# Kernel tuning notes

Measured on AMD Instinct MI355X. Metric: run time of the kernel, lower is better.

Reference implementation:

```python
import jax, jax.numpy as jnp
import numpy as np

B, S, D, H, NH = 128, 512, 64, 256, 8
HD = H // NH
NEG = -10000000000.0


def _ln(x, g, b, eps=1e-5):
    m = x.mean(-1, keepdims=True)
    v = ((x - m) ** 2).mean(-1, keepdims=True)
    return (x - m) * jax.lax.rsqrt(v + eps) * g + b


def _mha(xq, xkv, mask, qW, qb, kW, kb, vW, vb, oW, ob):
    # mask: [B,1,1,S_kv] bool, True = masked out
    b, sq, _ = xq.shape
    sk = xkv.shape[1]
    Q = (xq @ qW + qb).reshape(b, sq, NH, HD).transpose(0, 2, 1, 3)
    K = (xkv @ kW + kb).reshape(b, sk, NH, HD).transpose(0, 2, 1, 3)
    V = (xkv @ vW + vb).reshape(b, sk, NH, HD).transpose(0, 2, 1, 3)
    energy = jnp.einsum('bhqd,bhkd->bhqk', Q, K) / jnp.sqrt(jnp.float32(HD))
    energy = jnp.where(mask, NEG, energy)
    attn = jax.nn.softmax(energy, axis=-1)  # dropout is identity in eval
    x = jnp.einsum('bhqk,bhkd->bhqd', attn, V)
    x = x.transpose(0, 2, 1, 3).reshape(b, sq, H)
    return x @ oW + ob


def _ffn(x, f1W, f1b, f2W, f2b):
    # NewGELU == tanh-approximate GELU (GPT-2)
    return jax.nn.gelu(x @ f1W + f1b, approximate=True) @ f2W + f2b


def _fwd(src, ln0sg, ln0sb, ln0tg, ln0tb, semW, semb, temW, temb,
         e_qW, e_qb, e_kW, e_kb, e_vW, e_vb, e_oW, e_ob, e_ln1g, e_ln1b,
         e_f1W, e_f1b, e_f2W, e_f2b, e_ln2g, e_ln2b,
         d_sqW, d_sqb, d_skW, d_skb, d_svW, d_svb, d_soW, d_sob, d_ln1g, d_ln1b,
         d_eqW, d_eqb, d_ekW, d_ekb, d_evW, d_evb, d_eoW, d_eob, d_ln2g, d_ln2b,
         d_f1W, d_f1b, d_f2W, d_f2b, d_ln3g, d_ln3b, outW, outb):
    valid = src.sum(-1) != 0                      # [B,S] (prod_fea == 0)
    amask = (~valid)[:, None, None, :]            # [B,1,1,S]; trg==src so trg_mask==src_mask
    embs_src = _ln(src, ln0sg, ln0sb) @ semW + semb   # emb_need
    embs_trg = _ln(src, ln0tg, ln0tb) @ temW + temb
    # encoder layer
    a = _mha(embs_src, embs_src, amask, e_qW, e_qb, e_kW, e_kb, e_vW, e_vb, e_oW, e_ob)
    x = _ln(embs_src + a, e_ln1g, e_ln1b)
    enc_src = _ln(x + _ffn(x, e_f1W, e_f1b, e_f2W, e_f2b), e_ln2g, e_ln2b)
    # decoder layer
    a = _mha(embs_trg, embs_trg, amask, d_sqW, d_sqb, d_skW, d_skb, d_svW, d_svb, d_soW, d_sob)
    t = _ln(embs_trg + a, d_ln1g, d_ln1b)
    a = _mha(t, enc_src, amask, d_eqW, d_eqb, d_ekW, d_ekb, d_evW, d_evb, d_eoW, d_eob)
    t = _ln(t + a, d_ln2g, d_ln2b)
    t = _ln(t + _ffn(t, d_f1W, d_f1b, d_f2W, d_f2b), d_ln3g, d_ln3b)
    logits = (t @ outW + outb)[..., 0]            # [B,S]
    p = jnp.exp(logits) * valid.astype(logits.dtype)
    return p / p.sum(-1, keepdims=True)           # multi_purchase=False branch


def setup_inputs() -> dict:
    key = jax.random.key(0)
    keys = iter(jax.random.split(key, 64))
    inp = {"src": jax.random.normal(next(keys), (B, S, D), dtype=jnp.float32)}

    def lin(name, i, o):
        inp[name + "W"] = jax.random.normal(next(keys), (i, o), dtype=jnp.float32) * 0.02
        inp[name + "b"] = jnp.zeros((o,), dtype=jnp.float32)

    def ln(name, d):
        inp[name + "g"] = jnp.ones((d,), dtype=jnp.float32)
        inp[name + "b"] = jnp.zeros((d,), dtype=jnp.float32)

    ln("ln0s", D); ln("ln0t", D)
    lin("sem", D, H); lin("tem", D, H)
    for n in ["e_q", "e_k", "e_v", "e_o"]:
        lin(n, H, H)
    ln("e_ln1", H); lin("e_f1", H, H); lin("e_f2", H, H); ln("e_ln2", H)
    for n in ["d_sq", "d_sk", "d_sv", "d_so", "d_eq", "d_ek", "d_ev", "d_eo"]:
        lin(n, H, H)
    ln("d_ln1", H); ln("d_ln2", H)
    lin("d_f1", H, H); lin("d_f2", H, H); ln("d_ln3", H)
    lin("out", H, 1)
    return inp


def reference(src, ln0sg, ln0sb, ln0tg, ln0tb, semW, semb, temW, temb,
              e_qW, e_qb, e_kW, e_kb, e_vW, e_vb, e_oW, e_ob, e_ln1g, e_ln1b,
              e_f1W, e_f1b, e_f2W, e_f2b, e_ln2g, e_ln2b,
              d_sqW, d_sqb, d_skW, d_skb, d_svW, d_svb, d_soW, d_sob, d_ln1g, d_ln1b,
              d_eqW, d_eqb, d_ekW, d_ekb, d_evW, d_evb, d_eoW, d_eob, d_ln2g, d_ln2b,
              d_f1W, d_f1b, d_f2W, d_f2b, d_ln3g, d_ln3b, outW, outb):
    return _fwd(src, ln0sg, ln0sb, ln0tg, ln0tb, semW, semb, temW, temb,
                e_qW, e_qb, e_kW, e_kb, e_vW, e_vb, e_oW, e_ob, e_ln1g, e_ln1b,
                e_f1W, e_f1b, e_f2W, e_f2b, e_ln2g, e_ln2b,
                d_sqW, d_sqb, d_skW, d_skb, d_svW, d_svb, d_soW, d_sob, d_ln1g, d_ln1b,
                d_eqW, d_eqb, d_ekW, d_ekb, d_evW, d_evb, d_eoW, d_eob, d_ln2g, d_ln2b,
                d_f1W, d_f1b, d_f2W, d_f2b, d_ln3g, d_ln3b, outW, outb)
```

## Files before the change

### kernel.cpp

```cpp
#include <hip/hip_runtime.h>
#include <hip/hip_bf16.h>


#define Bb  128
#define Ss  512
#define Hh  256
#define NHh 8
#define Mm  (Bb*Ss)

typedef unsigned short bf16_t;
typedef __attribute__((ext_vector_type(8))) short short8;
typedef __attribute__((ext_vector_type(4))) float f32x4;

__device__ __forceinline__ float bf2f(bf16_t h){
  union { unsigned int u; float f; } v; v.u = ((unsigned int)h)<<16; return v.f;
}
__device__ __forceinline__ bf16_t f2bf(float f){
  union { float f; unsigned int u; } v; v.f = f;
  unsigned int r = (v.u + 0x7fffu + ((v.u>>16)&1u)) >> 16;
  return (bf16_t)r;
}
__device__ __forceinline__ unsigned pk_bf16(float a, float b){
  union { __hip_bfloat162 h; unsigned u; } v;
  v.h = __float22bfloat162_rn(float2{a,b});
  return v.u;
}
__device__ __forceinline__ short8 ld_bf8(const bf16_t* p){
  union { uint4 u; short8 s; } v; v.u = *(const uint4*)p; return v.s;
}
__device__ __forceinline__ void gload16(const bf16_t* g, bf16_t* l){
  __builtin_amdgcn_global_load_lds(
      (const __attribute__((address_space(1))) void*)g,
      (__attribute__((address_space(3))) void*)l, 16, 0, 0);
}
__device__ __forceinline__ float exp2_hw(float x){
  float r; asm("v_exp_f32 %0, %1" : "=v"(r) : "v"(x)); return r;
}
__device__ __forceinline__ float gelu_f(float x){
  float u = 0.7978845608028654f*(x + 0.044715f*x*x*x);
  float e = __expf(2.0f*u);
  float th = 1.0f - 2.0f*__builtin_amdgcn_rcpf(e + 1.0f);
  return 0.5f*x*(1.0f + th);
}

struct PrepDesc { const float* s; unsigned off; int K; };
struct Prep18  { PrepDesc d[18]; };

__global__ __launch_bounds__(256) void k_prep(Prep18 p, bf16_t* __restrict__ arena)
{
  PrepDesc dd = p.d[blockIdx.y];
  int i = blockIdx.x*256 + threadIdx.x;
  if (i < dd.K*256){
    int k = i>>8, n = i&255;
    arena[dd.off + n*dd.K + k] = f2bf(dd.s[i]);
  }
}

__global__ __launch_bounds__(256) void k_ln0(const float* __restrict__ src,
    const float* __restrict__ gs, const float* __restrict__ bs,
    const float* __restrict__ gt, const float* __restrict__ bt,
    bf16_t* __restrict__ xs, bf16_t* __restrict__ xt, float* __restrict__ valid)
{
  int row  = blockIdx.x*4 + (threadIdx.x>>6);
  int lane = threadIdx.x & 63;
  float x = src[(size_t)row*64 + lane];
  float s = x;
  #pragma unroll
  for (int o=32;o>0;o>>=1) s += __shfl_xor(s,o);
  float mean = s*(1.0f/64.0f);
  float d = x - mean;
  float ss = d*d;
  #pragma unroll
  for (int o=32;o>0;o>>=1) ss += __shfl_xor(ss,o);
  float r = rsqrtf(ss*(1.0f/64.0f) + 1e-5f);
  float xn = d*r;
  xs[(size_t)row*64+lane] = f2bf(xn*gs[lane] + bs[lane]);
  xt[(size_t)row*64+lane] = f2bf(xn*gt[lane] + bt[lane]);
  if (lane==0) valid[row] = (s != 0.0f) ? 1.0f : 0.0f;
}

struct GemmJob  { const bf16_t* A; const bf16_t* Wt; const float* bias; bf16_t* C;
                  int outm; float cs; };
struct GemmJobs { GemmJob j[3]; };

template<int KK>
__global__ __launch_bounds__(256,4) void k_gemm3(GemmJobs jobs)
{
  __shared__ bf16_t As[8*512];
  __shared__ bf16_t Bs[32*512];
  GemmJob jb = jobs.j[blockIdx.y];
  int t = threadIdx.x, w = t>>6, lane = t&63, l15 = lane&15, quad = lane>>4;
  int m0 = blockIdx.x*64;
  f32x4 z = {0.f,0.f,0.f,0.f};
  f32x4 acc[4][4] = {{z,z,z,z},{z,z,z,z},{z,z,z,z},{z,z,z,z}};

  #pragma unroll
  for (int k0=0; k0<KK; k0+=64){
    #pragma unroll
    for (int j=0; j<2; j++){
      int id = 2*w + j; int kc32 = id>>2, mt = id&3;
      gload16(jb.A + (size_t)(m0 + mt*16 + l15)*KK + k0 + kc32*32 + quad*8,
              &As[id*512]);
    }
    #pragma unroll
    for (int j=0; j<8; j++){
      int id = 8*w + j; int kc32 = id>>4, gnt = id&15;
      gload16(jb.Wt + (size_t)(gnt*16 + l15)*KK + k0 + kc32*32 + quad*8,
              &Bs[id*512]);
    }
    __syncthreads();
    #pragma unroll
    for (int kc=0; kc<2; kc++){
      short8 a[4], b[4];
      #pragma unroll
      for (int mt=0; mt<4; mt++) a[mt] = ld_bf8(&As[(kc*4+mt)*512 + lane*8]);
      #pragma unroll
      for (int nt=0; nt<4; nt++) b[nt] = ld_bf8(&Bs[(kc*16 + w*4 + nt)*512 + lane*8]);
      #pragma unroll
      for (int mt=0; mt<4; mt++)
        #pragma unroll
        for (int nt=0; nt<4; nt++)
          acc[mt][nt] = __builtin_amdgcn_mfma_f32_16x16x32_bf16(a[mt], b[nt], acc[mt][nt], 0,0,0);
    }
    __syncthreads();
  }

  float bv[4];
  #pragma unroll
  for (int nt=0; nt<4; nt++) bv[nt] = jb.bias[w*64 + nt*16 + l15];
  float cs = jb.cs;

  if (jb.outm == 0){
    #pragma unroll
    for (int mt=0; mt<4; mt++)
      #pragma unroll
      for (int nt=0; nt<4; nt++){
        int m = m0 + mt*16 + quad*4;
        int col = w*64 + nt*16 + l15;
        #pragma unroll
        for (int r=0; r<4; r++)
          jb.C[(size_t)(m+r)*256 + col] = f2bf((acc[mt][nt][r] + bv[nt])*cs);
      }
  } else {
    #pragma unroll
    for (int mt=0; mt<4; mt++)
      #pragma unroll
      for (int nt=0; nt<4; nt++){
        int m = m0 + mt*16 + quad*4;
        int col = w*64 + nt*16 + l15;
        uint2 pk = { pk_bf16(acc[mt][nt][0]+bv[nt], acc[mt][nt][1]+bv[nt]),
                     pk_bf16(acc[mt][nt][2]+bv[nt], acc[mt][nt][3]+bv[nt]) };
        *(uint2*)&jb.C[((size_t)((m>>9)*256 + col))*512 + (m&511)] = pk;
      }
  }
}

struct QkvJob { const bf16_t* A;
                const bf16_t* Wt0; const bf16_t* Wt1; const bf16_t* Wt2;
                const float* b0; const float* b1; const float* b2;
                bf16_t* C0; bf16_t* C1; bf16_t* C2; float qs; };

__global__ __launch_bounds__(256,2) void k_qkv(QkvJob jb)
{
  __shared__ bf16_t As[32*512];
  __shared__ bf16_t Bs[32*512];
  int t = threadIdx.x, w = t>>6, lane = t&63, l15 = lane&15, quad = lane>>4;
  int m0 = blockIdx.x*64;
  f32x4 z = {0.f,0.f,0.f,0.f};

  #pragma unroll
  for (int j=0; j<8; j++){
    int id = 8*w + j; int kc32 = id>>2, mt = id&3;
    gload16(jb.A + (size_t)(m0 + mt*16 + l15)*256 + kc32*32 + quad*8,
            &As[id*512]);
  }

  const bf16_t* Wts[3]  = { jb.Wt0, jb.Wt1, jb.Wt2 };
  const float*  bias[3] = { jb.b0,  jb.b1,  jb.b2  };
  bf16_t*       Cs[3]   = { jb.C0,  jb.C1,  jb.C2  };

  #pragma unroll 1
  for (int o=0; o<3; o++){
    const bf16_t* Wt = Wts[o];
    f32x4 acc[4][4] = {{z,z,z,z},{z,z,z,z},{z,z,z,z},{z,z,z,z}};
    #pragma unroll 1
    for (int ki=0; ki<4; ki++){
      #pragma unroll
      for (int j=0; j<8; j++){
        int id = 8*w + j; int kc32 = id>>4, gnt = id&15;
        gload16(Wt + (size_t)(gnt*16 + l15)*256 + ki*64 + kc32*32 + quad*8,
                &Bs[id*512]);
      }
      __syncthreads();
      #pragma unroll
      for (int kc=0; kc<2; kc++){
        short8 a[4], b[4];
        #pragma unroll
        for (int mt=0; mt<4; mt++)
          a[mt] = ld_bf8(&As[((ki*2+kc)*4 + mt)*512 + lane*8]);
        #pragma unroll
        for (int nt=0; nt<4; nt++)
          b[nt] = ld_bf8(&Bs[(kc*16 + w*4 + nt)*512 + lane*8]);
        #pragma unroll
        for (int mt=0; mt<4; mt++)
          #pragma unroll
          for (int nt=0; nt<4; nt++)
            acc[mt][nt] = __builtin_amdgcn_mfma_f32_16x16x32_bf16(a[mt], b[nt], acc[mt][nt], 0,0,0);
      }
      __syncthreads();
    }
    float bv[4];
    #pragma unroll
    for (int nt=0; nt<4; nt++) bv[nt] = bias[o][w*64 + nt*16 + l15];
    bf16_t* C = Cs[o];
    if (o < 2){
      float cs = (o==0) ? jb.qs : 1.0f;
      #pragma unroll
      for (int mt=0; mt<4; mt++)
        #pragma unroll
        for (int nt=0; nt<4; nt++){
          int m = m0 + mt*16 + quad*4;
          int col = w*64 + nt*16 + l15;
          #pragma unroll
          for (int r=0; r<4; r++)
            C[(size_t)(m+r)*256 + col] = f2bf((acc[mt][nt][r] + bv[nt])*cs);
        }
    } else {
      #pragma unroll
      for (int mt=0; mt<4; mt++)
        #pragma unroll
        for (int nt=0; nt<4; nt++){
          int m = m0 + mt*16 + quad*4;
          int col = w*64 + nt*16 + l15;
          uint2 pk = { pk_bf16(acc[mt][nt][0]+bv[nt], acc[mt][nt][1]+bv[nt]),
                       pk_bf16(acc[mt][nt][2]+bv[nt], acc[mt][nt][3]+bv[nt]) };
          *(uint2*)&C[((size_t)((m>>9)*256 + col))*512 + (m&511)] = pk;
        }
    }
  }
}

template<int EPI, int OUTM, int KK>
__global__ __launch_bounds__(256,4) void k_gemm(const bf16_t* __restrict__ A,
    const bf16_t* __restrict__ Wt, const float* __restrict__ bias,
    void* __restrict__ Cv, const bf16_t* __restrict__ Pres,
    const float* __restrict__ g, const float* __restrict__ bb,
    const float* __restrict__ oW, const float* __restrict__ obp)
{
  __shared__ bf16_t As[8*512];
  __shared__ bf16_t Bs[32*512];
  int t = threadIdx.x, w = t>>6, lane = t&63, l15 = lane&15, quad = lane>>4;
  int m0 = blockIdx.x*64;
  f32x4 z = {0.f,0.f,0.f,0.f};
  f32x4 acc[4][4] = {{z,z,z,z},{z,z,z,z},{z,z,z,z},{z,z,z,z}};

  #pragma unroll
  for (int k0=0; k0<KK; k0+=64){
    #pragma unroll
    for (int j=0; j<2; j++){
      int id = 2*w + j; int kc32 = id>>2, mt = id&3;
      gload16(A + (size_t)(m0 + mt*16 + l15)*KK + k0 + kc32*32 + quad*8,
              &As[id*512]);
    }
    #pragma unroll
    for (int j=0; j<8; j++){
      int id = 8*w + j; int kc32 = id>>4, gnt = id&15;
      gload16(Wt + (size_t)(gnt*16 + l15)*KK + k0 + kc32*32 + quad*8,
              &Bs[id*512]);
    }
    __syncthreads();
    #pragma unroll
    for (int kc=0; kc<2; kc++){
      short8 a[4], b[4];
      #pragma unroll
      for (int mt=0; mt<4; mt++) a[mt] = ld_bf8(&As[(kc*4+mt)*512 + lane*8]);
      #pragma unroll
      for (int nt=0; nt<4; nt++) b[nt] = ld_bf8(&Bs[(kc*16 + w*4 + nt)*512 + lane*8]);
      #pragma unroll
      for (int mt=0; mt<4; mt++)
        #pragma unroll
        for (int nt=0; nt<4; nt++)
          acc[mt][nt] = __builtin_amdgcn_mfma_f32_16x16x32_bf16(a[mt], b[nt], acc[mt][nt], 0,0,0);
    }
    __syncthreads();
  }

  float bv[4];
  #pragma unroll
  for (int nt=0; nt<4; nt++) bv[nt] = bias[w*64 + nt*16 + l15];

  if (OUTM==0){
    #pragma unroll
    for (int mt=0; mt<4; mt++)
      #pragma unroll
      for (int nt=0; nt<4; nt++)
        #pragma unroll
        for (int r=0; r<4; r++){
          int row = m0 + mt*16 + quad*4 + r;
          int col = w*64 + nt*16 + l15;
          float v = acc[mt][nt][r] + bv[nt];
          if (EPI==1) v = gelu_f(v);
          ((bf16_t*)Cv)[(size_t)row*256 + col] = f2bf(v);
        }
  } else {
    float* RedS = (float*)As;
    float* RedQ = RedS + 256;
    #pragma unroll
    for (int mt=0; mt<4; mt++)
      #pragma unroll
      for (int r=0; r<4; r++){
        int row = m0 + mt*16 + quad*4 + r;
        const bf16_t* pr = Pres + (size_t)row*256;
        float s = 0.f, q = 0.f;
        #pragma unroll
        for (int nt=0; nt<4; nt++){
          float v = acc[mt][nt][r] + bv[nt] + bf2f(pr[w*64 + nt*16 + l15]);
          s += v; q += v*v;
        }
        s += __shfl_xor(s,1); s += __shfl_xor(s,2);
        s += __shfl_xor(s,4); s += __shfl_xor(s,8);
        q += __shfl_xor(q,1); q += __shfl_xor(q,2);
        q += __shfl_xor(q,4); q += __shfl_xor(q,8);
        if (l15==0){
          int rr = mt*16 + quad*4 + r;
          RedS[rr*4 + w] = s; RedQ[rr*4 + w] = q;
        }
      }
    __syncthreads();

    float gv[4], bbv[4], wv[4];
    #pragma unroll
    for (int nt=0; nt<4; nt++){ gv[nt] = g[w*64+nt*16+l15]; bbv[nt] = bb[w*64+nt*16+l15]; }
    if (OUTM==5)
      #pragma unroll
      for (int nt=0; nt<4; nt++) wv[nt] = oW[w*64+nt*16+l15];

    float s2p[4][4];
    #pragma unroll
    for (int mt=0; mt<4; mt++)
      #pragma unroll
      for (int r=0; r<4; r++){
        int rr = mt*16 + quad*4 + r;
        int row = m0 + rr;
        float S = RedS[rr*4+0]+RedS[rr*4+1]+RedS[rr*4+2]+RedS[rr*4+3];
        float Q = RedQ[rr*4+0]+RedQ[rr*4+1]+RedQ[rr*4+2]+RedQ[rr*4+3];
        float mean = S*(1.0f/256.0f);
        float var  = Q*(1.0f/256.0f) - mean*mean;
        float rstd = rsqrtf(var + 1e-5f);
        const bf16_t* pr = Pres + (size_t)row*256;
        if (OUTM==3){
          bf16_t* po = (bf16_t*)Cv + (size_t)row*256;
          #pragma unroll
          for (int nt=0; nt<4; nt++){
            float v = acc[mt][nt][r] + bv[nt] + bf2f(pr[w*64 + nt*16 + l15]);
            po[w*64 + nt*16 + l15] = f2bf((v-mean)*rstd*gv[nt] + bbv[nt]);
          }
        } else {
          float s2 = 0.f;
          #pragma unroll
          for (int nt=0; nt<4; nt++){
            float v = acc[mt][nt][r] + bv[nt] + bf2f(pr[w*64 + nt*16 + l15]);
            s2 += ((v-mean)*rstd*gv[nt] + bbv[nt]) * wv[nt];
          }
          s2 += __shfl_xor(s2,1); s2 += __shfl_xor(s2,2);
          s2 += __shfl_xor(s2,4); s2 += __shfl_xor(s2,8);
          s2p[mt][r] = s2;
        }
      }
    if (OUTM==5){
      __syncthreads();
      #pragma unroll
      for (int mt=0; mt<4; mt++)
        #pragma unroll
        for (int r=0; r<4; r++)
          if (l15==0) RedS[(mt*16 + quad*4 + r)*4 + w] = s2p[mt][r];
      __syncthreads();
      if (w==0){
        float S = RedS[lane*4+0]+RedS[lane*4+1]+RedS[lane*4+2]+RedS[lane*4+3];
        ((float*)Cv)[m0 + lane] = S + obp[0];
      }
    }
  }
}

__global__ __launch_bounds__(256) void k_attn(const bf16_t* __restrict__ Qm,
    const bf16_t* __restrict__ Km, const bf16_t* __restrict__ VT,
    const float* __restrict__ valid, bf16_t* __restrict__ AO)
{
  __shared__ bf16_t Pbuf[4][2][2][16][40];
  __shared__ float  Smask[512];
  int t = threadIdx.x, wave = t>>6, lane = t&63, l15 = lane&15, quad = lane>>4;
  int lid = blockIdx.x + 8*blockIdx.y + 1024*blockIdx.z;
  int hp = lid & 3, pb = (lid>>2)&1, g = (lid>>3)&7, bh = lid>>6;
  int h  = hp*2 + (g&1);
  int qc = g>>1;
  int b  = bh*2 + pb;
  int q0 = qc*128;

  Smask[t]     = (valid[b*Ss + t      ] != 0.f) ? 0.f : -1.44269504e10f;
  Smask[t+256] = (valid[b*Ss + t + 256] != 0.f) ? 0.f : -1.44269504e10f;
  __syncthreads();

  short8 aQ0 = ld_bf8(Qm + (size_t)(b*Ss + q0 + (wave*2  )*16 + l15)*256 + h*32 + quad*8);
  short8 aQ1 = ld_bf8(Qm + (size_t)(b*Ss + q0 + (wave*2+1)*16 + l15)*256 + h*32 + quad*8);
  const bf16_t* Kb = Km + (size_t)(b*Ss)*256 + h*32;
  const bf16_t* Vb = VT + ((size_t)b*256 + h*32)*512;

  f32x4 z = {0.f,0.f,0.f,0.f};
  f32x4 O0[2] = {z,z}, O1[2] = {z,z};
  float ls0 = 0.f, ls1 = 0.f;

  auto process = [&](int kt2n, short8 K0, short8 K1){
    int s = kt2n & 1;
    #pragma unroll
    for (int half=0; half<2; half++){
      short8 aK = half ? K1 : K0;
      int ktile = kt2n*2 + half;
      __builtin_amdgcn_s_setprio(1);
      f32x4 s0 = __builtin_amdgcn_mfma_f32_16x16x32_bf16(aK, aQ0, z, 0,0,0);
      f32x4 s1 = __builtin_amdgcn_mfma_f32_16x16x32_bf16(aK, aQ1, z, 0,0,0);
      __builtin_amdgcn_s_setprio(0);
      float4 mb = *(const float4*)&Smask[ktile*16 + quad*4];
      float p00 = exp2_hw(s0[0] + mb.x);
      float p01 = exp2_hw(s0[1] + mb.y);
      float p02 = exp2_hw(s0[2] + mb.z);
      float p03 = exp2_hw(s0[3] + mb.w);
      float p10 = exp2_hw(s1[0] + mb.x);
      float p11 = exp2_hw(s1[1] + mb.y);
      float p12 = exp2_hw(s1[2] + mb.z);
      float p13 = exp2_hw(s1[3] + mb.w);
      ls0 += (p00+p01)+(p02+p03);
      ls1 += (p10+p11)+(p12+p13);
      uint2 w0 = { pk_bf16(p00,p01), pk_bf16(p02,p03) };
      uint2 w1 = { pk_bf16(p10,p11), pk_bf16(p12,p13) };
      *(uint2*)&Pbuf[wave][0][s][l15][half*16 + quad*4] = w0;
      *(uint2*)&Pbuf[wave][1][s][l15][half*16 + quad*4] = w1;
    }
  };
  auto loadK = [&](int n, short8& K0, short8& K1){
    K0 = ld_bf8(Kb + (size_t)((n*2  )*16 + l15)*256 + quad*8);
    K1 = ld_bf8(Kb + (size_t)((n*2+1)*16 + l15)*256 + quad*8);
  };
  auto loadV = [&](int n, short8& V0, short8& V1){
    V0 = ld_bf8(Vb + (size_t)(l15   )*512 + n*32 + quad*8);
    V1 = ld_bf8(Vb + (size_t)(16+l15)*512 + n*32 + quad*8);
  };

  short8 cK0, cK1, pK0, pK1, nK0, nK1;
  short8 cV0, cV1, mV0, mV1, nV0, nV1;
  loadK(0, cK0, cK1);
  process(0, cK0, cK1);
  loadK(1, pK0, pK1);
  loadV(0, cV0, cV1);
  loadV(1, mV0, mV1);

  #pragma unroll 2
  for (int kt2=0; kt2<16; kt2++){
    if (kt2+2 < 16){ loadK(kt2+2, nK0, nK1); loadV(kt2+2, nV0, nV1); }
    int s = kt2 & 1;
    short8 aP0 = ld_bf8(&Pbuf[wave][0][s][l15][quad*8]);
    short8 aP1 = ld_bf8(&Pbuf[wave][1][s][l15][quad*8]);
    __builtin_amdgcn_s_setprio(1);
    O0[0] = __builtin_amdgcn_mfma_f32_16x16x32_bf16(aP0, cV0, O0[0], 0,0,0);
    O0[1] = __builtin_amdgcn_mfma_f32_16x16x32_bf16(aP0, cV1, O0[1], 0,0,0);
    O1[0] = __builtin_amdgcn_mfma_f32_16x16x32_bf16(aP1, cV0, O1[0], 0,0,0);
    O1[1] = __builtin_amdgcn_mfma_f32_16x16x32_bf16(aP1, cV1, O1[1], 0,0,0);
    __builtin_amdgcn_s_setprio(0);
    if (kt2+1 < 16) process(kt2+1, pK0, pK1);
    pK0 = nK0; pK1 = nK1;
    cV0 = mV0; cV1 = mV1; mV0 = nV0; mV1 = nV1;
  }

  ls0 += __shfl_xor(ls0,16); ls0 += __shfl_xor(ls0,32);
  ls1 += __shfl_xor(ls1,16); ls1 += __shfl_xor(ls1,32);
  float linv0 = (ls0 > 0.f) ? 1.0f/ls0 : 0.f;
  float linv1 = (ls1 > 0.f) ? 1.0f/ls1 : 0.f;
  float i0[4], i1[4];
  #pragma unroll
  for (int r=0; r<4; r++){
    i0[r] = __shfl(linv0, quad*4 + r);
    i1[r] = __shfl(linv1, quad*4 + r);
  }
  size_t r0 = (size_t)(b*Ss + q0 + (wave*2  )*16);
  size_t r1 = (size_t)(b*Ss + q0 + (wave*2+1)*16);
  #pragma unroll
  for (int nt=0; nt<2; nt++)
    #pragma unroll
    for (int r=0; r<4; r++){
      AO[(r0 + quad*4 + r)*256 + h*32 + nt*16 + l15] = f2bf(O0[nt][r]*i0[r]);
      AO[(r1 + quad*4 + r)*256 + h*32 + nt*16 + l15] = f2bf(O1[nt][r]*i1[r]);
    }
}

__global__ __launch_bounds__(256) void k_final(const float* __restrict__ L,
    const float* __restrict__ valid, float* __restrict__ out)
{
  __shared__ float wsum[4];
  int b = blockIdx.x, t = threadIdx.x;
  float e0 = __expf(L[b*Ss + t      ]) * valid[b*Ss + t      ];
  float e1 = __expf(L[b*Ss + 256 + t]) * valid[b*Ss + 256 + t];
  float s = e0 + e1;
  #pragma unroll
  for (int o=32;o>0;o>>=1) s += __shfl_xor(s,o);
  if ((t&63)==0) wsum[t>>6] = s;
  __syncthreads();
  float tot = wsum[0]+wsum[1]+wsum[2]+wsum[3];
  out[b*Ss + t      ] = e0/tot;
  out[b*Ss + 256 + t] = e1/tot;
}

extern "C" void kernel_launch(void* const* d_in, const int* in_sizes, int n_in,
                              void* d_out, int out_size, void* d_ws, size_t ws_size,
                              hipStream_t stream)
{
  #define F(i) ((const float*)d_in[(i)])
  bool sig = (in_sizes[33] == 256);
  const float* d_eqW  = F(sig?35:33); const float* d_eqb  = F(sig?36:34);
  const float* d_ekW  = F(sig?37:35); const float* d_ekb  = F(sig?38:36);
  const float* d_evW  = F(sig?39:37); const float* d_evb  = F(sig?40:38);
  const float* d_eoW  = F(sig?41:39); const float* d_eob  = F(sig?42:40);
  const float* d_ln1g = F(sig?33:41); const float* d_ln1b = F(sig?34:42);

  char* w = (char*)d_ws;
  bf16_t* P0 = (bf16_t*)w; w += (size_t)Mm*Hh*2;
  bf16_t* P1 = (bf16_t*)w; w += (size_t)Mm*Hh*2;
  bf16_t* H0 = (bf16_t*)w; w += (size_t)Mm*Hh*2;
  bf16_t* H1 = (bf16_t*)w;
  bf16_t* xs = (bf16_t*)w; w += (size_t)Mm*Hh*2;
  bf16_t* H2 = (bf16_t*)w;
  bf16_t* xt = (bf16_t*)w; w += (size_t)Mm*Hh*2;
  bf16_t* Wa = (bf16_t*)w; w += (size_t)(2*16384 + 16*65536)*2;
  float*  valid  = (float*)w; w += (size_t)Mm*4;
  float*  logits = (float*)w; w += (size_t)Mm*4;
  float* out = (float*)d_out;

  unsigned o_sem = 0, o_tem = 16384;
  unsigned o_w[16]; for (int i=0;i<16;i++) o_w[i] = 32768 + i*65536u;
  Prep18 pp;
  const float* srcs[18] = { F(5), F(7), F(9), F(11), F(13), F(15), F(19), F(21),
                            F(25), F(27), F(29), F(31), d_eqW, d_ekW, d_evW, d_eoW,
                            F(45), F(47) };
  unsigned offs[18] = { o_sem, o_tem, o_w[0],o_w[1],o_w[2],o_w[3],o_w[4],o_w[5],
                        o_w[6],o_w[7],o_w[8],o_w[9],o_w[10],o_w[11],o_w[12],o_w[13],
                        o_w[14],o_w[15] };
  for (int i=0;i<18;i++){ pp.d[i].s = srcs[i]; pp.d[i].off = offs[i]; pp.d[i].K = (i<2)?64:256; }

  dim3 blk(256);
  dim3 gLN(Mm/4);
  dim3 gG(Mm/64);
  dim3 gA(NHh, Bb, 4);
  dim3 gP(256, 18);
  const float* NF = nullptr; const bf16_t* NB = nullptr;
  const float QS = 0.17677669529663687f * 1.4426950408889634f;

  k_prep<<<gP, blk, 0, stream>>>(pp, Wa);
  k_ln0<<<gLN, blk, 0, stream>>>(F(0), F(1),F(2), F(3),F(4), xs, xt, valid);

  {
    GemmJobs js;
    js.j[0] = { xs, Wa+o_sem, F(6), P0, 0, 1.0f };
    js.j[1] = { xt, Wa+o_tem, F(8), P1, 0, 1.0f };
    js.j[2] = js.j[0];
    k_gemm3<64><<<dim3(Mm/64,2), blk, 0, stream>>>(js);
  }

  auto QJ = [&](const bf16_t* A, int wq, int wk, int wv,
                const float* bq, const float* bk, const float* bv2,
                const bf16_t* Ak){
    QkvJob j; j.A = A;
    j.Wt0 = Wa+o_w[wq]; j.Wt1 = Wa+o_w[wk]; j.Wt2 = Wa+o_w[wv];
    j.b0 = bq; j.b1 = bk; j.b2 = bv2;
    j.C0 = H0; j.C1 = H1; j.C2 = H2; j.qs = QS;
    (void)Ak; return j;
  };

  {
    QkvJob j = QJ(P0, 0,1,2, F(10),F(12),F(14), P0);
    k_qkv<<<gG, blk, 0, stream>>>(j);
  }
  k_attn<<<gA, blk, 0, stream>>>(H0, H1, H2, valid, H0);
  k_gemm<0,3,256><<<gG, blk, 0, stream>>>(H0, Wa+o_w[3], F(16), P0, P0, F(17),F(18), NF,NF);
  k_gemm<1,0,256><<<gG, blk, 0, stream>>>(P0, Wa+o_w[4], F(20), H0, NB,NF,NF,NF,NF);
  k_gemm<0,3,256><<<gG, blk, 0, stream>>>(H0, Wa+o_w[5], F(22), P0, P0, F(23),F(24), NF,NF);

  {
    QkvJob j = QJ(P1, 6,7,8, F(26),F(28),F(30), P1);
    k_qkv<<<gG, blk, 0, stream>>>(j);
  }
  k_attn<<<gA, blk, 0, stream>>>(H0, H1, H2, valid, H0);
  k_gemm<0,3,256><<<gG, blk, 0, stream>>>(H0, Wa+o_w[9], F(32), P1, P1, d_ln1g,d_ln1b, NF,NF);

  {
    k_gemm<0,0,256><<<gG, blk, 0, stream>>>(P1, Wa+o_w[10], d_eqb, H0, NB,NF,NF,NF,NF);
    GemmJobs js;
    js.j[0] = { P0, Wa+o_w[11], d_ekb, H1, 0, 1.0f };
    js.j[1] = { P0, Wa+o_w[12], d_evb, H2, 2, 1.0f };
    js.j[2] = js.j[0];
    k_gemm3<256><<<dim3(Mm/64,2), blk, 0, stream>>>(js);
  }
  k_attn<<<gA, blk, 0, stream>>>(H0, H1, H2, valid, H0);
  k_gemm<0,3,256><<<gG, blk, 0, stream>>>(H0, Wa+o_w[13], d_eob, P1, P1, F(43),F(44), NF,NF);

  k_gemm<1,0,256><<<gG, blk, 0, stream>>>(P1, Wa+o_w[14], F(46), H0, NB,NF,NF,NF,NF);
  k_gemm<0,5,256><<<gG, blk, 0, stream>>>(H0, Wa+o_w[15], F(48), logits, P1, F(49),F(50), F(51),F(52));

  k_final<<<dim3(Bb), blk, 0, stream>>>(logits, valid, out);
  #undef F
}
```

Baseline: 1.020 ms.

## Use 128-row GEMM tiles with 512-thread blocks to share weight tiles

Doubles the M tile of the generic and triple-job GEMM kernels from 64 to 128 rows and runs them with 8 waves per block, arranged as 2 row halves by 4 column groups. Each 256-wide weight tile loaded into shared memory is now reused across twice as many rows, which halves weight traffic per output row and halves the grid size. The fused residual+LayerNorm and logit epilogues are reworked to reduce across the new wave layout. Block-level occupancy and register limits change with the 512-thread launch bounds.

```diff
diff --git a/kernel.cpp b/kernel.cpp
--- a/kernel.cpp
+++ b/kernel.cpp
@@ -84,13 +84,14 @@
 struct GemmJobs { GemmJob j[3]; };
 
 template<int KK>
-__global__ __launch_bounds__(256,4) void k_gemm3(GemmJobs jobs)
-{
-  __shared__ bf16_t As[8*512];
+__global__ __launch_bounds__(512,6) void k_gemm3(GemmJobs jobs)
+{
+  __shared__ bf16_t As[16*512];
   __shared__ bf16_t Bs[32*512];
   GemmJob jb = jobs.j[blockIdx.y];
   int t = threadIdx.x, w = t>>6, lane = t&63, l15 = lane&15, quad = lane>>4;
-  int m0 = blockIdx.x*64;
+  int wh = w>>2, wn = w&3;
+  int m0 = blockIdx.x*128;
   f32x4 z = {0.f,0.f,0.f,0.f};
   f32x4 acc[4][4] = {{z,z,z,z},{z,z,z,z},{z,z,z,z},{z,z,z,z}};
 
@@ -98,13 +99,13 @@
   for (int k0=0; k0<KK; k0+=64){
     #pragma unroll
     for (int j=0; j<2; j++){
-      int id = 2*w + j; int kc32 = id>>2, mt = id&3;
-      gload16(jb.A + (size_t)(m0 + mt*16 + l15)*KK + k0 + kc32*32 + quad*8,
+      int id = 2*w + j; int h = id>>3, kc32 = (id>>2)&1, mt = id&3;
+      gload16(jb.A + (size_t)(m0 + h*64 + mt*16 + l15)*KK + k0 + kc32*32 + quad*8,
               &As[id*512]);
     }
     #pragma unroll
-    for (int j=0; j<8; j++){
-      int id = 8*w + j; int kc32 = id>>4, gnt = id&15;
+    for (int j=0; j<4; j++){
+      int id = 4*w + j; int kc32 = id>>4, gnt = id&15;
       gload16(jb.Wt + (size_t)(gnt*16 + l15)*KK + k0 + kc32*32 + quad*8,
               &Bs[id*512]);
     }
@@ -113,9 +114,9 @@
     for (int kc=0; kc<2; kc++){
       short8 a[4], b[4];
       #pragma unroll
-      for (int mt=0; mt<4; mt++) a[mt] = ld_bf8(&As[(kc*4+mt)*512 + lane*8]);
-      #pragma unroll
-      for (int nt=0; nt<4; nt++) b[nt] = ld_bf8(&Bs[(kc*16 + w*4 + nt)*512 + lane*8]);
+      for (int mt=0; mt<4; mt++) a[mt] = ld_bf8(&As[(wh*8 + kc*4 + mt)*512 + lane*8]);
+      #pragma unroll
+      for (int nt=0; nt<4; nt++) b[nt] = ld_bf8(&Bs[(kc*16 + wn*4 + nt)*512 + lane*8]);
       #pragma unroll
       for (int mt=0; mt<4; mt++)
         #pragma unroll
@@ -127,7 +128,7 @@
 
   float bv[4];
   #pragma unroll
-  for (int nt=0; nt<4; nt++) bv[nt] = jb.bias[w*64 + nt*16 + l15];
+  for (int nt=0; nt<4; nt++) bv[nt] = jb.bias[wn*64 + nt*16 + l15];
   float cs = jb.cs;
 
   if (jb.outm == 0){
@@ -135,8 +136,8 @@
     for (int mt=0; mt<4; mt++)
       #pragma unroll
       for (int nt=0; nt<4; nt++){
-        int m = m0 + mt*16 + quad*4;
-        int col = w*64 + nt*16 + l15;
+        int m = m0 + wh*64 + mt*16 + quad*4;
+        int col = wn*64 + nt*16 + l15;
         #pragma unroll
         for (int r=0; r<4; r++)
           jb.C[(size_t)(m+r)*256 + col] = f2bf((acc[mt][nt][r] + bv[nt])*cs);
@@ -146,8 +147,8 @@
     for (int mt=0; mt<4; mt++)
       #pragma unroll
       for (int nt=0; nt<4; nt++){
-        int m = m0 + mt*16 + quad*4;
-        int col = w*64 + nt*16 + l15;
+        int m = m0 + wh*64 + mt*16 + quad*4;
+        int col = wn*64 + nt*16 + l15;
         uint2 pk = { pk_bf16(acc[mt][nt][0]+bv[nt], acc[mt][nt][1]+bv[nt]),
                      pk_bf16(acc[mt][nt][2]+bv[nt], acc[mt][nt][3]+bv[nt]) };
         *(uint2*)&jb.C[((size_t)((m>>9)*256 + col))*512 + (m&511)] = pk;
@@ -241,16 +242,17 @@
 }
 
 template<int EPI, int OUTM, int KK>
-__global__ __launch_bounds__(256,4) void k_gemm(const bf16_t* __restrict__ A,
+__global__ __launch_bounds__(512,6) void k_gemm(const bf16_t* __restrict__ A,
     const bf16_t* __restrict__ Wt, const float* __restrict__ bias,
     void* __restrict__ Cv, const bf16_t* __restrict__ Pres,
     const float* __restrict__ g, const float* __restrict__ bb,
     const float* __restrict__ oW, const float* __restrict__ obp)
 {
-  __shared__ bf16_t As[8*512];
+  __shared__ bf16_t As[16*512];
   __shared__ bf16_t Bs[32*512];
   int t = threadIdx.x, w = t>>6, lane = t&63, l15 = lane&15, quad = lane>>4;
-  int m0 = blockIdx.x*64;
+  int wh = w>>2, wn = w&3;
+  int m0 = blockIdx.x*128;
   f32x4 z = {0.f,0.f,0.f,0.f};
   f32x4 acc[4][4] = {{z,z,z,z},{z,z,z,z},{z,z,z,z},{z,z,z,z}};
 
@@ -258,13 +260,13 @@
   for (int k0=0; k0<KK; k0+=64){
     #pragma unroll
     for (int j=0; j<2; j++){
-      int id = 2*w + j; int kc32 = id>>2, mt = id&3;
-      gload16(A + (size_t)(m0 + mt*16 + l15)*KK + k0 + kc32*32 + quad*8,
+      int id = 2*w + j; int h = id>>3, kc32 = (id>>2)&1, mt = id&3;
+      gload16(A + (size_t)(m0 + h*64 + mt*16 + l15)*KK + k0 + kc32*32 + quad*8,
               &As[id*512]);
     }
     #pragma unroll
-    for (int j=0; j<8; j++){
-      int id = 8*w + j; int kc32 = id>>4, gnt = id&15;
+    for (int j=0; j<4; j++){
+      int id = 4*w + j; int kc32 = id>>4, gnt = id&15;
       gload16(Wt + (size_t)(gnt*16 + l15)*KK + k0 + kc32*32 + quad*8,
               &Bs[id*512]);
     }
@@ -273,9 +275,9 @@
     for (int kc=0; kc<2; kc++){
       short8 a[4], b[4];
       #pragma unroll
-      for (int mt=0; mt<4; mt++) a[mt] = ld_bf8(&As[(kc*4+mt)*512 + lane*8]);
-      #pragma unroll
-      for (int nt=0; nt<4; nt++) b[nt] = ld_bf8(&Bs[(kc*16 + w*4 + nt)*512 + lane*8]);
+      for (int mt=0; mt<4; mt++) a[mt] = ld_bf8(&As[(wh*8 + kc*4 + mt)*512 + lane*8]);
+      #pragma unroll
+      for (int nt=0; nt<4; nt++) b[nt] = ld_bf8(&Bs[(kc*16 + wn*4 + nt)*512 + lane*8]);
       #pragma unroll
       for (int mt=0; mt<4; mt++)
         #pragma unroll
@@ -287,7 +289,7 @@
 
   float bv[4];
   #pragma unroll
-  for (int nt=0; nt<4; nt++) bv[nt] = bias[w*64 + nt*16 + l15];
+  for (int nt=0; nt<4; nt++) bv[nt] = bias[wn*64 + nt*16 + l15];
 
   if (OUTM==0){
     #pragma unroll
@@ -296,51 +298,49 @@
       for (int nt=0; nt<4; nt++)
         #pragma unroll
         for (int r=0; r<4; r++){
-          int row = m0 + mt*16 + quad*4 + r;
-          int col = w*64 + nt*16 + l15;
+          int row = m0 + wh*64 + mt*16 + quad*4 + r;
+          int col = wn*64 + nt*16 + l15;
           float v = acc[mt][nt][r] + bv[nt];
           if (EPI==1) v = gelu_f(v);
           ((bf16_t*)Cv)[(size_t)row*256 + col] = f2bf(v);
         }
   } else {
     float* RedS = (float*)As;
-    float* RedQ = RedS + 256;
+    float* RedQ = RedS + 512;
     #pragma unroll
     for (int mt=0; mt<4; mt++)
       #pragma unroll
       for (int r=0; r<4; r++){
-        int row = m0 + mt*16 + quad*4 + r;
+        int rr = wh*64 + mt*16 + quad*4 + r;
+        int row = m0 + rr;
         const bf16_t* pr = Pres + (size_t)row*256;
         float s = 0.f, q = 0.f;
         #pragma unroll
         for (int nt=0; nt<4; nt++){
-          float v = acc[mt][nt][r] + bv[nt] + bf2f(pr[w*64 + nt*16 + l15]);
+          float v = acc[mt][nt][r] + bv[nt] + bf2f(pr[wn*64 + nt*16 + l15]);
           s += v; q += v*v;
         }
         s += __shfl_xor(s,1); s += __shfl_xor(s,2);
         s += __shfl_xor(s,4); s += __shfl_xor(s,8);
         q += __shfl_xor(q,1); q += __shfl_xor(q,2);
         q += __shfl_xor(q,4); q += __shfl_xor(q,8);
-        if (l15==0){
-          int rr = mt*16 + quad*4 + r;
-          RedS[rr*4 + w] = s; RedQ[rr*4 + w] = q;
-        }
+        if (l15==0){ RedS[rr*4 + wn] = s; RedQ[rr*4 + wn] = q; }
       }
     __syncthreads();
 
     float gv[4], bbv[4], wv[4];
     #pragma unroll
-    for (int nt=0; nt<4; nt++){ gv[nt] = g[w*64+nt*16+l15]; bbv[nt] = bb[w*64+nt*16+l15]; }
+    for (int nt=0; nt<4; nt++){ gv[nt] = g[wn*64+nt*16+l15]; bbv[nt] = bb[wn*64+nt*16+l15]; }
     if (OUTM==5)
       #pragma unroll
-      for (int nt=0; nt<4; nt++) wv[nt] = oW[w*64+nt*16+l15];
+      for (int nt=0; nt<4; nt++) wv[nt] = oW[wn*64+nt*16+l15];
 
     float s2p[4][4];
     #pragma unroll
     for (int mt=0; mt<4; mt++)
       #pragma unroll
       for (int r=0; r<4; r++){
-        int rr = mt*16 + quad*4 + r;
+        int rr = wh*64 + mt*16 + quad*4 + r;
         int row = m0 + rr;
         float S = RedS[rr*4+0]+RedS[rr*4+1]+RedS[rr*4+2]+RedS[rr*4+3];
         float Q = RedQ[rr*4+0]+RedQ[rr*4+1]+RedQ[rr*4+2]+RedQ[rr*4+3];
@@ -352,14 +352,14 @@
           bf16_t* po = (bf16_t*)Cv + (size_t)row*256;
           #pragma unroll
           for (int nt=0; nt<4; nt++){
-            float v = acc[mt][nt][r] + bv[nt] + bf2f(pr[w*64 + nt*16 + l15]);
-            po[w*64 + nt*16 + l15] = f2bf((v-mean)*rstd*gv[nt] + bbv[nt]);
+            float v = acc[mt][nt][r] + bv[nt] + bf2f(pr[wn*64 + nt*16 + l15]);
+            po[wn*64 + nt*16 + l15] = f2bf((v-mean)*rstd*gv[nt] + bbv[nt]);
           }
         } else {
           float s2 = 0.f;
           #pragma unroll
           for (int nt=0; nt<4; nt++){
-            float v = acc[mt][nt][r] + bv[nt] + bf2f(pr[w*64 + nt*16 + l15]);
+            float v = acc[mt][nt][r] + bv[nt] + bf2f(pr[wn*64 + nt*16 + l15]);
             s2 += ((v-mean)*rstd*gv[nt] + bbv[nt]) * wv[nt];
           }
           s2 += __shfl_xor(s2,1); s2 += __shfl_xor(s2,2);
@@ -373,11 +373,12 @@
       for (int mt=0; mt<4; mt++)
         #pragma unroll
         for (int r=0; r<4; r++)
-          if (l15==0) RedS[(mt*16 + quad*4 + r)*4 + w] = s2p[mt][r];
+          if (l15==0) RedS[(wh*64 + mt*16 + quad*4 + r)*4 + wn] = s2p[mt][r];
       __syncthreads();
-      if (w==0){
-        float S = RedS[lane*4+0]+RedS[lane*4+1]+RedS[lane*4+2]+RedS[lane*4+3];
-        ((float*)Cv)[m0 + lane] = S + obp[0];
+      if (w < 2){
+        int rr = w*64 + lane;
+        float S = RedS[rr*4+0]+RedS[rr*4+1]+RedS[rr*4+2]+RedS[rr*4+3];
+        ((float*)Cv)[m0 + rr] = S + obp[0];
       }
     }
   }
@@ -546,8 +547,10 @@
   for (int i=0;i<18;i++){ pp.d[i].s = srcs[i]; pp.d[i].off = offs[i]; pp.d[i].K = (i<2)?64:256; }
 
   dim3 blk(256);
+  dim3 blk512(512);
   dim3 gLN(Mm/4);
   dim3 gG(Mm/64);
+  dim3 gG2(Mm/128);
   dim3 gA(NHh, Bb, 4);
   dim3 gP(256, 18);
   const float* NF = nullptr; const bf16_t* NB = nullptr;
@@ -561,7 +564,7 @@
     js.j[0] = { xs, Wa+o_sem, F(6), P0, 0, 1.0f };
     js.j[1] = { xt, Wa+o_tem, F(8), P1, 0, 1.0f };
     js.j[2] = js.j[0];
-    k_gemm3<64><<<dim3(Mm/64,2), blk, 0, stream>>>(js);
+    k_gemm3<64><<<dim3(Mm/128,2), blk512, 0, stream>>>(js);
   }
 
   auto QJ = [&](const bf16_t* A, int wq, int wk, int wv,
@@ -579,30 +582,30 @@
     k_qkv<<<gG, blk, 0, stream>>>(j);
   }
   k_attn<<<gA, blk, 0, stream>>>(H0, H1, H2, valid, H0);
-  k_gemm<0,3,256><<<gG, blk, 0, stream>>>(H0, Wa+o_w[3], F(16), P0, P0, F(17),F(18), NF,NF);
-  k_gemm<1,0,256><<<gG, blk, 0, stream>>>(P0, Wa+o_w[4], F(20), H0, NB,NF,NF,NF,NF);
-  k_gemm<0,3,256><<<gG, blk, 0, stream>>>(H0, Wa+o_w[5], F(22), P0, P0, F(23),F(24), NF,NF);
+  k_gemm<0,3,256><<<gG2, blk512, 0, stream>>>(H0, Wa+o_w[3], F(16), P0, P0, F(17),F(18), NF,NF);
+  k_gemm<1,0,256><<<gG2, blk512, 0, stream>>>(P0, Wa+o_w[4], F(20), H0, NB,NF,NF,NF,NF);
+  k_gemm<0,3,256><<<gG2, blk512, 0, stream>>>(H0, Wa+o_w[5], F(22), P0, P0, F(23),F(24), NF,NF);
 
   {
     QkvJob j = QJ(P1, 6,7,8, F(26),F(28),F(30), P1);
     k_qkv<<<gG, blk, 0, stream>>>(j);
   }
   k_attn<<<gA, blk, 0, stream>>>(H0, H1, H2, valid, H0);
-  k_gemm<0,3,256><<<gG, blk, 0, stream>>>(H0, Wa+o_w[9], F(32), P1, P1, d_ln1g,d_ln1b, NF,NF);
+  k_gemm<0,3,256><<<gG2, blk512, 0, stream>>>(H0, Wa+o_w[9], F(32), P1, P1, d_ln1g,d_ln1b, NF,NF);
 
   {
-    k_gemm<0,0,256><<<gG, blk, 0, stream>>>(P1, Wa+o_w[10], d_eqb, H0, NB,NF,NF,NF,NF);
+    k_gemm<0,0,256><<<gG2, blk512, 0, stream>>>(P1, Wa+o_w[10], d_eqb, H0, NB,NF,NF,NF,NF);
     GemmJobs js;
     js.j[0] = { P0, Wa+o_w[11], d_ekb, H1, 0, 1.0f };
     js.j[1] = { P0, Wa+o_w[12], d_evb, H2, 2, 1.0f };
     js.j[2] = js.j[0];
-    k_gemm3<256><<<dim3(Mm/64,2), blk, 0, stream>>>(js);
+    k_gemm3<256><<<dim3(Mm/128,2), blk512, 0, stream>>>(js);
   }
   k_attn<<<gA, blk, 0, stream>>>(H0, H1, H2, valid, H0);
-  k_gemm<0,3,256><<<gG, blk, 0, stream>>>(H0, Wa+o_w[13], d_eob, P1, P1, F(43),F(44), NF,NF);
-
-  k_gemm<1,0,256><<<gG, blk, 0, stream>>>(P1, Wa+o_w[14], F(46), H0, NB,NF,NF,NF,NF);
-  k_gemm<0,5,256><<<gG, blk, 0, stream>>>(H0, Wa+o_w[15], F(48), logits, P1, F(49),F(50), F(51),F(52));
+  k_gemm<0,3,256><<<gG2, blk512, 0, stream>>>(H0, Wa+o_w[13], d_eob, P1, P1, F(43),F(44), NF,NF);
+
+  k_gemm<1,0,256><<<gG2, blk512, 0, stream>>>(P1, Wa+o_w[14], F(46), H0, NB,NF,NF,NF,NF);
+  k_gemm<0,5,256><<<gG2, blk512, 0, stream>>>(H0, Wa+o_w[15], F(48), logits, P1, F(49),F(50), F(51),F(52));
 
   k_final<<<dim3(Bb), blk, 0, stream>>>(logits, valid, out);
   #undef F
```

New measurement: 1.847 ms. 1.81x slower.
